# Optimization experiments

Measured on AMD Instinct MI355X. Metric: run time of the kernel, lower is better.

Reference implementation:

```python
import jax, jax.numpy as jnp
import numpy as np
from functools import partial

N_MAX = 10
M = 10
T = 0.5
SQRT_T = T ** 0.5
HIDDEN = 2048
LATENT = 128
STROKE = 5
B = 128
INPUT_DIM = LATENT + STROKE  # 133
OUT_DIM = 6 * M + 3          # 63


def setup_inputs() -> dict:
    key = jax.random.key(0)
    ks = jax.random.split(key, 10)
    def init(k, shape, fan_in):
        return jax.random.normal(k, shape, dtype=jnp.float32) * (1.0 / np.sqrt(fan_in))
    return {
        "z": jax.random.normal(ks[0], (B, LATENT), dtype=jnp.float32),
        "N_s": jax.random.randint(ks[1], (B,), 0, N_MAX),
        "fc_in_w": init(ks[2], (2 * HIDDEN, LATENT), LATENT),
        "fc_in_b": jnp.zeros((2 * HIDDEN,), jnp.float32),
        "W_ih": init(ks[3], (4 * HIDDEN, INPUT_DIM), INPUT_DIM),
        "W_hh": init(ks[4], (4 * HIDDEN, HIDDEN), HIDDEN),
        "b_ih": jnp.zeros((4 * HIDDEN,), jnp.float32),
        "b_hh": jnp.zeros((4 * HIDDEN,), jnp.float32),
        "proj_w": init(ks[5], (OUT_DIM, HIDDEN), HIDDEN),
        "proj_b": jnp.zeros((OUT_DIM,), jnp.float32),
    }


def reference(z, N_s, fc_in_w, fc_in_b, W_ih, W_hh, b_ih, b_hh, proj_w, proj_b):
    # initial hidden/cell from latent: tanh(fc_in(z)) split into (h, c)
    hc = jnp.tanh(z @ fc_in_w.T + fc_in_b)          # (B, 2H)
    h0, c0 = hc[:, :HIDDEN], hc[:, HIDDEN:]
    keys = jax.random.split(jax.random.key(42), N_MAX)
    stroke0 = jnp.tile(jnp.array([0., 0., 1., 0., 0.], z.dtype), (B, 1))
    empty = jnp.array([0., 0., 0., 0., 1.], z.dtype)
    eye3 = jnp.eye(3, dtype=z.dtype)

    def step(carry, inp):
        h, c, stroke = carry
        i, key = inp
        # ---- LSTM cell (PyTorch gate order i,f,g,o) ----
        x = jnp.concatenate([z, stroke], axis=1)                     # (B, 133)
        gates = x @ W_ih.T + b_ih + h @ W_hh.T + b_hh                # (B, 4H)
        ig, fg, gg, og = jnp.split(gates, 4, axis=1)
        c_new = jax.nn.sigmoid(fg) * c + jax.nn.sigmoid(ig) * jnp.tanh(gg)
        h_new = jax.nn.sigmoid(og) * jnp.tanh(c_new)
        out = h_new @ proj_w.T + proj_b                              # (B, 63)
        # ---- MDN parameter extraction ----
        mix = out[:, :6 * M].reshape(B, M, 6)                        # (B, M, 6)
        pi = jax.nn.softmax(mix[:, :, 0] / T, axis=1)                # (B, M)
        mux, muy = mix[:, :, 1], mix[:, :, 2]
        sx = jnp.exp(mix[:, :, 3]) * SQRT_T
        sy = jnp.exp(mix[:, :, 4]) * SQRT_T
        rho = jnp.tanh(mix[:, :, 5])
        pen = jax.nn.softmax(out[:, 6 * M:] / T, axis=1)             # (B, 3)
        # ---- categorical sampling via cumsum + searchsorted ----
        k1, k2, k3, k4 = jax.random.split(key, 4)
        u = jax.random.uniform(k1, (B,), dtype=z.dtype)
        rx = jax.random.normal(k2, (B,), dtype=z.dtype)
        ry = jax.random.normal(k3, (B,), dtype=z.dtype)
        u2 = jax.random.uniform(k4, (B,), dtype=z.dtype)
        idx = jnp.clip(jnp.sum(jnp.cumsum(pi, axis=1) < u[:, None], axis=1), 0, M - 1)
        take = lambda a: jnp.take_along_axis(a, idx[:, None], axis=1)[:, 0]
        mx, my = take(mux), take(muy)
        sxg, syg, rg = take(sx), take(sy), take(rho)
        ox = mx + sxg * rx
        oy = my + syg * (rg * ox + jnp.sqrt(1.0 - rg ** 2) * ry)
        pidx = jnp.clip(jnp.sum(jnp.cumsum(pen, axis=1) < u2[:, None], axis=1), 0, 2)
        nxt = jnp.concatenate([ox[:, None], oy[:, None], eye3[pidx]], axis=1)  # (B, 5)
        # finished sequences emit the empty stroke
        nxt = jnp.where((i > N_s)[:, None], empty, nxt)
        return (h_new, c_new, nxt), nxt

    _, strokes = jax.lax.scan(step, (h0, c0, stroke0), (jnp.arange(N_MAX), keys))
    return strokes  # (N_max, B, stroke_dim)
```

## Files before the change

### kernel.cpp

```cpp
#include <hip/hip_runtime.h>
#include <stdint.h>
#include <stddef.h>

#define HID 2048
#define NB 128
#define NG 8192
#define ODIM 63

typedef unsigned int u32;
typedef unsigned short u16;
typedef short bf16x8 __attribute__((ext_vector_type(8)));
typedef float f32x4 __attribute__((ext_vector_type(4)));

__device__ __forceinline__ u16 f2bf(float x) {
  u32 u = __float_as_uint(x);
  return (u16)((u + 0x7FFFu + ((u >> 16) & 1u)) >> 16);
}
__device__ __forceinline__ float bf2f(u16 b) {
  return __uint_as_float(((u32)b) << 16);
}

__device__ __forceinline__ void tf2x32(u32 k0, u32 k1, u32 x0, u32 x1,
                                       u32& o0, u32& o1) {
  u32 ks2 = k0 ^ k1 ^ 0x1BD11BDAu;
  x0 += k0; x1 += k1;
#define TF_ROTL(v,d) (((v)<<(d))|((v)>>(32-(d))))
#define TF_R(r) { x0 += x1; x1 = TF_ROTL(x1,r); x1 ^= x0; }
  TF_R(13) TF_R(15) TF_R(26) TF_R(6)
  x0 += k1;  x1 += ks2 + 1u;
  TF_R(17) TF_R(29) TF_R(16) TF_R(24)
  x0 += ks2; x1 += k0 + 2u;
  TF_R(13) TF_R(15) TF_R(26) TF_R(6)
  x0 += k0;  x1 += k1 + 3u;
  TF_R(17) TF_R(29) TF_R(16) TF_R(24)
  x0 += k1;  x1 += ks2 + 4u;
  TF_R(13) TF_R(15) TF_R(26) TF_R(6)
  x0 += ks2; x1 += k0 + 5u;
  o0 = x0; o1 = x1;
#undef TF_R
#undef TF_ROTL
}

__device__ __forceinline__ float unif01(u32 b) {
  return __uint_as_float((b >> 9) | 0x3f800000u) - 1.0f;
}

__device__ __forceinline__ float erfinv_xla(float x) {
  float t = x * x;
  float w = -log1pf(-t);
  float p;
  if (w < 5.0f) {
    w = w - 2.5f;
    p = 2.81022636e-08f;
    p = fmaf(p, w, 3.43273939e-07f);
    p = fmaf(p, w, -3.5233877e-06f);
    p = fmaf(p, w, -4.39150654e-06f);
    p = fmaf(p, w, 0.00021858087f);
    p = fmaf(p, w, -0.00125372503f);
    p = fmaf(p, w, -0.00417768164f);
    p = fmaf(p, w, 0.246640727f);
    p = fmaf(p, w, 1.50140941f);
  } else {
    w = sqrtf(w) - 3.0f;
    p = -0.000200214257f;
    p = fmaf(p, w, 0.000100950558f);
    p = fmaf(p, w, 0.00134934322f);
    p = fmaf(p, w, -0.00367342844f);
    p = fmaf(p, w, 0.00573950773f);
    p = fmaf(p, w, -0.0076224613f);
    p = fmaf(p, w, 0.00943887047f);
    p = fmaf(p, w, 1.00167406f);
    p = fmaf(p, w, 2.83297682f);
  }
  return p * x;
}

__device__ __forceinline__ float norm_from_bits(u32 b) {
  float f = unif01(b);
  float v = f * 2.0f + __uint_as_float(0xBF7FFFFFu);
  return __uint_as_float(0x3FB504F3u) * erfinv_xla(v);
}

__global__ void rand_kernel(float* __restrict__ u, float* __restrict__ rx,
                            float* __restrict__ ry, float* __restrict__ u2,
                            float* __restrict__ stroke) {
  const int i = blockIdx.x;
  const int l = threadIdx.x;
  if (i == 0) {
    stroke[l*5+0] = 0.f; stroke[l*5+1] = 0.f; stroke[l*5+2] = 1.f;
    stroke[l*5+3] = 0.f; stroke[l*5+4] = 0.f;
  }
  u32 ki0, ki1;
  tf2x32(0u, 42u, 0u, (u32)i, ki0, ki1);
  u32 k1a,k1b,k2a,k2b,k3a,k3b,k4a,k4b;
  tf2x32(ki0, ki1, 0u, 0u, k1a, k1b);
  tf2x32(ki0, ki1, 0u, 1u, k2a, k2b);
  tf2x32(ki0, ki1, 0u, 2u, k3a, k3b);
  tf2x32(ki0, ki1, 0u, 3u, k4a, k4b);
  u32 o0, o1;
  const u32 ul = (u32)l;
  tf2x32(k1a, k1b, 0u, ul, o0, o1);  u [i*NB + l] = unif01(o0 ^ o1);
  tf2x32(k2a, k2b, 0u, ul, o0, o1);  rx[i*NB + l] = norm_from_bits(o0 ^ o1);
  tf2x32(k3a, k3b, 0u, ul, o0, o1);  ry[i*NB + l] = norm_from_bits(o0 ^ o1);
  tf2x32(k4a, k4b, 0u, ul, o0, o1);  u2[i*NB + l] = unif01(o0 ^ o1);
}

__global__ __launch_bounds__(256) void w_split(const float* __restrict__ W,
                                               u16* __restrict__ Whi,
                                               u16* __restrict__ Wlo) {
  const int i8 = (blockIdx.x * 256 + threadIdx.x) * 8;
  float4 v0 = *(const float4*)&W[i8];
  float4 v1 = *(const float4*)&W[i8 + 4];
  float v[8] = {v0.x, v0.y, v0.z, v0.w, v1.x, v1.y, v1.z, v1.w};
  u32 hp[4], lp[4];
#pragma unroll
  for (int j = 0; j < 4; ++j) {
    u16 h0 = f2bf(v[2*j]),   l0 = f2bf(v[2*j]   - bf2f(h0));
    u16 h1 = f2bf(v[2*j+1]), l1 = f2bf(v[2*j+1] - bf2f(h1));
    hp[j] = (u32)h0 | ((u32)h1 << 16);
    lp[j] = (u32)l0 | ((u32)l1 << 16);
  }
  *(uint4*)&Whi[i8] = make_uint4(hp[0], hp[1], hp[2], hp[3]);
  *(uint4*)&Wlo[i8] = make_uint4(lp[0], lp[1], lp[2], lp[3]);
}

#define BM 64
#define BN 64
#define BK 16
__global__ __launch_bounds__(256) void gemm_bt(
    const float* __restrict__ A, const float* __restrict__ B,
    int K, int ldb, int N, int mode,
    const float* __restrict__ bias1, const float* __restrict__ bias2,
    float* __restrict__ C, float* __restrict__ C2,
    u16* __restrict__ Chi, u16* __restrict__ Clo)
{
  __shared__ float As[BK][BM];
  __shared__ float Bs[BK][BN];
  const int tid = threadIdx.x;
  const int bm = blockIdx.y * BM;
  const int bn = blockIdx.x * BN;
  const int lr = tid >> 2;
  const int lk = (tid & 3) << 2;
  const int ty = tid >> 4, tx = tid & 15;
  const int mo = ty << 2, no = tx << 2;
  const bool b_aligned = ((ldb & 3) == 0);
  float acc[4][4] = {{0.f,0.f,0.f,0.f},{0.f,0.f,0.f,0.f},{0.f,0.f,0.f,0.f},{0.f,0.f,0.f,0.f}};

  for (int k0 = 0; k0 < K; k0 += BK) {
    const float* ap = A + (size_t)(bm + lr) * K + (k0 + lk);
    float4 av = *(const float4*)ap;
    As[lk+0][lr] = av.x; As[lk+1][lr] = av.y; As[lk+2][lr] = av.z; As[lk+3][lr] = av.w;
    const float* bp = B + (size_t)(bn + lr) * ldb + (k0 + lk);
    float4 bv;
    if (b_aligned) { bv = *(const float4*)bp; }
    else { bv.x = bp[0]; bv.y = bp[1]; bv.z = bp[2]; bv.w = bp[3]; }
    Bs[lk+0][lr] = bv.x; Bs[lk+1][lr] = bv.y; Bs[lk+2][lr] = bv.z; Bs[lk+3][lr] = bv.w;
    __syncthreads();
#pragma unroll
    for (int k = 0; k < BK; ++k) {
      float4 a = *(const float4*)&As[k][mo];
      float4 b = *(const float4*)&Bs[k][no];
      acc[0][0] = fmaf(a.x, b.x, acc[0][0]);
      acc[0][1] = fmaf(a.x, b.y, acc[0][1]);
      acc[0][2] = fmaf(a.x, b.z, acc[0][2]);
      acc[0][3] = fmaf(a.x, b.w, acc[0][3]);
      acc[1][0] = fmaf(a.y, b.x, acc[1][0]);
      acc[1][1] = fmaf(a.y, b.y, acc[1][1]);
      acc[1][2] = fmaf(a.y, b.z, acc[1][2]);
      acc[1][3] = fmaf(a.y, b.w, acc[1][3]);
      acc[2][0] = fmaf(a.z, b.x, acc[2][0]);
      acc[2][1] = fmaf(a.z, b.y, acc[2][1]);
      acc[2][2] = fmaf(a.z, b.z, acc[2][2]);
      acc[2][3] = fmaf(a.z, b.w, acc[2][3]);
      acc[3][0] = fmaf(a.w, b.x, acc[3][0]);
      acc[3][1] = fmaf(a.w, b.y, acc[3][1]);
      acc[3][2] = fmaf(a.w, b.z, acc[3][2]);
      acc[3][3] = fmaf(a.w, b.w, acc[3][3]);
    }
    __syncthreads();
  }

  const int n0 = bn + no;
#pragma unroll
  for (int i = 0; i < 4; ++i) {
    const int m = bm + mo + i;
    if (mode == 1) {
      float4 r;
      r.x = tanhf(acc[i][0] + bias1[n0+0]);
      r.y = tanhf(acc[i][1] + bias1[n0+1]);
      r.z = tanhf(acc[i][2] + bias1[n0+2]);
      r.w = tanhf(acc[i][3] + bias1[n0+3]);
      if (n0 < HID) {
        *(float4*)&C[(size_t)m * HID + n0] = r;
        if (Chi) {
          float rv[4] = {r.x, r.y, r.z, r.w};
          u32 hp[2], lp[2];
#pragma unroll
          for (int j = 0; j < 2; ++j) {
            u16 h0 = f2bf(rv[2*j]),   l0 = f2bf(rv[2*j]   - bf2f(h0));
            u16 h1 = f2bf(rv[2*j+1]), l1 = f2bf(rv[2*j+1] - bf2f(h1));
            hp[j] = (u32)h0 | ((u32)h1 << 16);
            lp[j] = (u32)l0 | ((u32)l1 << 16);
          }
          *(uint2*)&Chi[(size_t)m * HID + n0] = make_uint2(hp[0], hp[1]);
          *(uint2*)&Clo[(size_t)m * HID + n0] = make_uint2(lp[0], lp[1]);
        }
      } else {
        *(float4*)&C2[(size_t)m * HID + (n0-HID)] = r;
      }
    } else {
      float4 r;
      r.x = acc[i][0] + bias1[n0+0] + bias2[n0+0];
      r.y = acc[i][1] + bias1[n0+1] + bias2[n0+1];
      r.z = acc[i][2] + bias1[n0+2] + bias2[n0+2];
      r.w = acc[i][3] + bias1[n0+3] + bias2[n0+3];
      *(float4*)&C[(size_t)m * N + n0] = r;
    }
  }
}

__global__ __launch_bounds__(256) void rec_mfma_lstm(
    const u16* __restrict__ hHi, const u16* __restrict__ hLo,
    const u16* __restrict__ WHi, const u16* __restrict__ WLo,
    const float* __restrict__ gz,
    const float* __restrict__ W_ih,
    const float* __restrict__ stroke,
    float* __restrict__ c,
    float* __restrict__ h_next,
    u16* __restrict__ hHiN, u16* __restrict__ hLoN)
{
  __shared__ float gt[4][32][33];
  const int tid = threadIdx.x;
  const int jc = blockIdx.x;
  const int mb = blockIdx.y;
  const int g  = tid >> 6;
  const int l  = tid & 63;
  const int lr = l & 15;
  const int lk = (l >> 4) * 8;

  f32x4 acc00 = {0.f,0.f,0.f,0.f}, acc01 = {0.f,0.f,0.f,0.f};
  f32x4 acc10 = {0.f,0.f,0.f,0.f}, acc11 = {0.f,0.f,0.f,0.f};

  const u16* pa0h = hHi + (size_t)(mb*32 +      lr) * HID + lk;
  const u16* pa1h = hHi + (size_t)(mb*32 + 16 + lr) * HID + lk;
  const u16* pa0l = hLo + (size_t)(mb*32 +      lr) * HID + lk;
  const u16* pa1l = hLo + (size_t)(mb*32 + 16 + lr) * HID + lk;
  const size_t bn0 = (size_t)(g*HID + jc*32 +      lr) * HID + lk;
  const size_t bn1 = (size_t)(g*HID + jc*32 + 16 + lr) * HID + lk;
  const u16* pb0h = WHi + bn0;
  const u16* pb1h = WHi + bn1;
  const u16* pb0l = WLo + bn0;
  const u16* pb1l = WLo + bn1;

#pragma unroll 2
  for (int k0 = 0; k0 < HID; k0 += 32) {
    bf16x8 a0h = *(const bf16x8*)(pa0h + k0);
    bf16x8 a1h = *(const bf16x8*)(pa1h + k0);
    bf16x8 a0l = *(const bf16x8*)(pa0l + k0);
    bf16x8 a1l = *(const bf16x8*)(pa1l + k0);
    bf16x8 b0h = *(const bf16x8*)(pb0h + k0);
    bf16x8 b1h = *(const bf16x8*)(pb1h + k0);
    bf16x8 b0l = *(const bf16x8*)(pb0l + k0);
    bf16x8 b1l = *(const bf16x8*)(pb1l + k0);
    acc00 = __builtin_amdgcn_mfma_f32_16x16x32_bf16(a0h, b0h, acc00, 0, 0, 0);
    acc00 = __builtin_amdgcn_mfma_f32_16x16x32_bf16(a0h, b0l, acc00, 0, 0, 0);
    acc00 = __builtin_amdgcn_mfma_f32_16x16x32_bf16(a0l, b0h, acc00, 0, 0, 0);
    acc01 = __builtin_amdgcn_mfma_f32_16x16x32_bf16(a0h, b1h, acc01, 0, 0, 0);
    acc01 = __builtin_amdgcn_mfma_f32_16x16x32_bf16(a0h, b1l, acc01, 0, 0, 0);
    acc01 = __builtin_amdgcn_mfma_f32_16x16x32_bf16(a0l, b1h, acc01, 0, 0, 0);
    acc10 = __builtin_amdgcn_mfma_f32_16x16x32_bf16(a1h, b0h, acc10, 0, 0, 0);
    acc10 = __builtin_amdgcn_mfma_f32_16x16x32_bf16(a1h, b0l, acc10, 0, 0, 0);
    acc10 = __builtin_amdgcn_mfma_f32_16x16x32_bf16(a1l, b0h, acc10, 0, 0, 0);
    acc11 = __builtin_amdgcn_mfma_f32_16x16x32_bf16(a1h, b1h, acc11, 0, 0, 0);
    acc11 = __builtin_amdgcn_mfma_f32_16x16x32_bf16(a1h, b1l, acc11, 0, 0, 0);
    acc11 = __builtin_amdgcn_mfma_f32_16x16x32_bf16(a1l, b1h, acc11, 0, 0, 0);
  }

  {
    const int rr = (l >> 4) * 4;
#pragma unroll
    for (int r = 0; r < 4; ++r) {
      gt[g][ 0 + rr + r][ 0 + lr] = acc00[r];
      gt[g][ 0 + rr + r][16 + lr] = acc01[r];
      gt[g][16 + rr + r][ 0 + lr] = acc10[r];
      gt[g][16 + rr + r][16 + lr] = acc11[r];
    }
  }
  __syncthreads();

  const int m  = tid >> 3;
  const int j4 = (tid & 7) * 4;
  const int gm = mb*32 + m;
  const int col = jc*32 + j4;
  float gv[4][4];
#pragma unroll
  for (int q = 0; q < 4; ++q) {
    float4 z4 = *(const float4*)&gz[(size_t)gm * NG + q * HID + col];
    gv[q][0] = z4.x + gt[q][m][j4+0];
    gv[q][1] = z4.y + gt[q][m][j4+1];
    gv[q][2] = z4.z + gt[q][m][j4+2];
    gv[q][3] = z4.w + gt[q][m][j4+3];
  }
  const float* st = stroke + gm*5;
  float s0 = st[0], s1 = st[1], s2 = st[2], s3 = st[3], s4 = st[4];
#pragma unroll
  for (int q = 0; q < 4; ++q) {
#pragma unroll
    for (int i = 0; i < 4; ++i) {
      const float* w = W_ih + (size_t)(q * HID + col + i) * 133 + 128;
      float t0 = gv[q][i];
      t0 = fmaf(s0, w[0], t0);
      t0 = fmaf(s1, w[1], t0);
      t0 = fmaf(s2, w[2], t0);
      t0 = fmaf(s3, w[3], t0);
      t0 = fmaf(s4, w[4], t0);
      gv[q][i] = t0;
    }
  }
  const size_t cidx = (size_t)gm * HID + col;
  float4 cv = *(float4*)&c[cidx];
  float cin[4] = {cv.x, cv.y, cv.z, cv.w};
  float hn[4], cn[4];
#pragma unroll
  for (int i = 0; i < 4; ++i) {
    float ig = 1.0f / (1.0f + expf(-gv[0][i]));
    float fg = 1.0f / (1.0f + expf(-gv[1][i]));
    float gg = tanhf(gv[2][i]);
    float og = 1.0f / (1.0f + expf(-gv[3][i]));
    cn[i] = fg * cin[i] + ig * gg;
    hn[i] = og * tanhf(cn[i]);
  }
  *(float4*)&c[cidx]      = make_float4(cn[0], cn[1], cn[2], cn[3]);
  *(float4*)&h_next[cidx] = make_float4(hn[0], hn[1], hn[2], hn[3]);
  u32 hp[2], lp[2];
#pragma unroll
  for (int j = 0; j < 2; ++j) {
    u16 h0 = f2bf(hn[2*j]),   l0 = f2bf(hn[2*j]   - bf2f(h0));
    u16 h1 = f2bf(hn[2*j+1]), l1 = f2bf(hn[2*j+1] - bf2f(h1));
    hp[j] = (u32)h0 | ((u32)h1 << 16);
    lp[j] = (u32)l0 | ((u32)l1 << 16);
  }
  *(uint2*)&hHiN[cidx] = make_uint2(hp[0], hp[1]);
  *(uint2*)&hLoN[cidx] = make_uint2(lp[0], lp[1]);
}

#define BK2 32
__global__ __launch_bounds__(256) void rec_gemm_lstm(
    const float* __restrict__ A, const float* __restrict__ W,
    const float* __restrict__ gz, const float* __restrict__ W_ih,
    const float* __restrict__ stroke, float* __restrict__ c,
    float* __restrict__ h_next)
{
  __shared__ float As[2][BK2][64];
  __shared__ float Bs[2][BK2][64];
  __shared__ float gt[64][68];
  const int tid = threadIdx.x;
  const int jc = blockIdx.x;
  const int bm = blockIdx.y * 64;
  const int j0 = jc * 16;
  const int sr = tid & 63;
  const int sk = (tid >> 6) << 3;
  const int brow = (sr >> 4) * HID + j0 + (sr & 15);
  const int mo = (tid >> 4) << 2;
  const int no = (tid & 15) << 2;
  float acc[4][4] = {{0.f,0.f,0.f,0.f},{0.f,0.f,0.f,0.f},{0.f,0.f,0.f,0.f},{0.f,0.f,0.f,0.f}};
  const float* abase = A + (size_t)(bm + sr) * HID + sk;
  const float* bbase = W + (size_t)brow * HID + sk;
#define STG(bi) do { \
    As[bi][sk+0][sr]=ra0.x; As[bi][sk+1][sr]=ra0.y; As[bi][sk+2][sr]=ra0.z; As[bi][sk+3][sr]=ra0.w; \
    As[bi][sk+4][sr]=ra1.x; As[bi][sk+5][sr]=ra1.y; As[bi][sk+6][sr]=ra1.z; As[bi][sk+7][sr]=ra1.w; \
    Bs[bi][sk+0][sr]=rb0.x; Bs[bi][sk+1][sr]=rb0.y; Bs[bi][sk+2][sr]=rb0.z; Bs[bi][sk+3][sr]=rb0.w; \
    Bs[bi][sk+4][sr]=rb1.x; Bs[bi][sk+5][sr]=rb1.y; Bs[bi][sk+6][sr]=rb1.z; Bs[bi][sk+7][sr]=rb1.w; \
  } while (0)
  float4 ra0 = *(const float4*)(abase);
  float4 ra1 = *(const float4*)(abase + 4);
  float4 rb0 = *(const float4*)(bbase);
  float4 rb1 = *(const float4*)(bbase + 4);
  STG(0);
  __syncthreads();
  int cur = 0;
  for (int t = 0; t < 64; ++t) {
    if (t < 63) {
      ra0 = *(const float4*)(abase + (t+1)*BK2);
      ra1 = *(const float4*)(abase + (t+1)*BK2 + 4);
      rb0 = *(const float4*)(bbase + (t+1)*BK2);
      rb1 = *(const float4*)(bbase + (t+1)*BK2 + 4);
    }
#pragma unroll
    for (int k = 0; k < BK2; ++k) {
      float4 a = *(const float4*)&As[cur][k][mo];
      float4 b = *(const float4*)&Bs[cur][k][no];
      acc[0][0] = fmaf(a.x, b.x, acc[0][0]);
      acc[0][1] = fmaf(a.x, b.y, acc[0][1]);
      acc[0][2] = fmaf(a.x, b.z, acc[0][2]);
      acc[0][3] = fmaf(a.x, b.w, acc[0][3]);
      acc[1][0] = fmaf(a.y, b.x, acc[1][0]);
      acc[1][1] = fmaf(a.y, b.y, acc[1][1]);
      acc[1][2] = fmaf(a.y, b.z, acc[1][2]);
      acc[1][3] = fmaf(a.y, b.w, acc[1][3]);
      acc[2][0] = fmaf(a.z, b.x, acc[2][0]);
      acc[2][1] = fmaf(a.z, b.y, acc[2][1]);
      acc[2][2] = fmaf(a.z, b.z, acc[2][2]);
      acc[2][3] = fmaf(a.z, b.w, acc[2][3]);
      acc[3][0] = fmaf(a.w, b.x, acc[3][0]);
      acc[3][1] = fmaf(a.w, b.y, acc[3][1]);
      acc[3][2] = fmaf(a.w, b.z, acc[3][2]);
      acc[3][3] = fmaf(a.w, b.w, acc[3][3]);
    }
    if (t < 63) STG(cur ^ 1);
    __syncthreads();
    cur ^= 1;
  }
#undef STG
  const int g = no >> 4;
#pragma unroll
  for (int i = 0; i < 4; ++i) {
    const int m = mo + i;
    float4 gzv = *(const float4*)&gz[(size_t)(bm + m) * NG + g * HID + j0 + (no & 15)];
    gt[m][no+0] = acc[i][0] + gzv.x;
    gt[m][no+1] = acc[i][1] + gzv.y;
    gt[m][no+2] = acc[i][2] + gzv.z;
    gt[m][no+3] = acc[i][3] + gzv.w;
  }
  __syncthreads();
#pragma unroll
  for (int p = 0; p < 4; ++p) {
    const int pid = p * 256 + tid;
    const int m  = pid >> 4;
    const int jj = pid & 15;
    const int gm = bm + m;
    const int col = j0 + jj;
    float gv[4];
    gv[0] = gt[m][jj];
    gv[1] = gt[m][16+jj];
    gv[2] = gt[m][32+jj];
    gv[3] = gt[m][48+jj];
    const float* st = stroke + gm*5;
    float s0 = st[0], s1 = st[1], s2 = st[2], s3 = st[3], s4 = st[4];
#pragma unroll
    for (int q = 0; q < 4; ++q) {
      const float* w = W_ih + (size_t)(q * HID + col) * 133 + 128;
      float t0 = gv[q];
      t0 = fmaf(s0, w[0], t0);
      t0 = fmaf(s1, w[1], t0);
      t0 = fmaf(s2, w[2], t0);
      t0 = fmaf(s3, w[3], t0);
      t0 = fmaf(s4, w[4], t0);
      gv[q] = t0;
    }
    float ig = 1.0f / (1.0f + expf(-gv[0]));
    float fg = 1.0f / (1.0f + expf(-gv[1]));
    float gg = tanhf(gv[2]);
    float og = 1.0f / (1.0f + expf(-gv[3]));
    const size_t idx = (size_t)gm * HID + col;
    float cn = fg * c[idx] + ig * gg;
    float hnv = og * tanhf(cn);
    c[idx] = cn;
    h_next[idx] = hnv;
  }
}

__global__ __launch_bounds__(256) void projsample(
    const float* __restrict__ h, const float* __restrict__ pw,
    const float* __restrict__ pb, const int* __restrict__ N_s,
    const float* __restrict__ u, const float* __restrict__ rx,
    const float* __restrict__ ry, const float* __restrict__ u2, int step,
    float* __restrict__ stroke, float* __restrict__ dout)
{
  __shared__ float hl[4*520];
  __shared__ float outs[64];
  const int b = blockIdx.x;
  const int t = threadIdx.x;
  const float* hp = h + (size_t)b * HID;
  {
    const int part = t >> 6;
    const int kk = (t * 8) & 511;
    float4 v0 = *(const float4*)&hp[t*8];
    float4 v1 = *(const float4*)&hp[t*8+4];
    *(float4*)&hl[part*520 + kk]     = v0;
    *(float4*)&hl[part*520 + kk + 4] = v1;
  }
  __syncthreads();
  if (t < 252) {
    const int n = t >> 2, part = t & 3;
    const float* wrow = pw + (size_t)n * HID + part * 512;
    const float* hh = hl + part * 520;
    float acc = 0.f;
#pragma unroll 4
    for (int k = 0; k < 512; k += 4) {
      float4 wv = *(const float4*)&wrow[k];
      float4 hv = *(const float4*)&hh[k];
      acc = fmaf(hv.x, wv.x, acc);
      acc = fmaf(hv.y, wv.y, acc);
      acc = fmaf(hv.z, wv.z, acc);
      acc = fmaf(hv.w, wv.w, acc);
    }
    acc += __shfl_xor(acc, 1);
    acc += __shfl_xor(acc, 2);
    if (part == 0) outs[n] = acc + pb[n];
  }
  __syncthreads();
  if (t == 0) {
    const float* o = outs;
    float xs[10];
    float mx = -3.402823466e+38f;
#pragma unroll
    for (int m = 0; m < 10; ++m) { xs[m] = o[6*m] * 2.0f; mx = fmaxf(mx, xs[m]); }
    float e[10]; float ssum = 0.f;
#pragma unroll
    for (int m = 0; m < 10; ++m) { e[m] = expf(xs[m] - mx); ssum += e[m]; }
    float uu = u[b];
    int cnt = 0; float csum = 0.f;
#pragma unroll
    for (int m = 0; m < 10; ++m) { csum += e[m] / ssum; cnt += (csum < uu) ? 1 : 0; }
    int idx = cnt > 9 ? 9 : cnt;
    float mux = o[6*idx+1], muy = o[6*idx+2];
    float sxg = expf(o[6*idx+3]) * __uint_as_float(0x3F3504F3u);
    float syg = expf(o[6*idx+4]) * __uint_as_float(0x3F3504F3u);
    float rg  = tanhf(o[6*idx+5]);
    float ox = mux + sxg * rx[b];
    float oy = muy + syg * (rg * ox + sqrtf(1.0f - rg*rg) * ry[b]);
    float p0 = o[60]*2.0f, p1 = o[61]*2.0f, p2 = o[62]*2.0f;
    float pmx = fmaxf(p0, fmaxf(p1, p2));
    float e0 = expf(p0-pmx), e1 = expf(p1-pmx), e2 = expf(p2-pmx);
    float es = e0+e1+e2;
    float uu2 = u2[b];
    int c2 = 0; float cs = 0.f;
    cs += e0/es; c2 += (cs < uu2) ? 1 : 0;
    cs += e1/es; c2 += (cs < uu2) ? 1 : 0;
    cs += e2/es; c2 += (cs < uu2) ? 1 : 0;
    int pidx = c2 > 2 ? 2 : c2;
    float nx0 = ox, nx1 = oy;
    float nx2 = (pidx==0)?1.f:0.f, nx3 = (pidx==1)?1.f:0.f, nx4 = (pidx==2)?1.f:0.f;
    if (step > N_s[b]) { nx0=0.f; nx1=0.f; nx2=0.f; nx3=0.f; nx4=1.f; }
    float* sp = stroke + b*5;
    sp[0]=nx0; sp[1]=nx1; sp[2]=nx2; sp[3]=nx3; sp[4]=nx4;
    float* dp = dout + b*5;
    dp[0]=nx0; dp[1]=nx1; dp[2]=nx2; dp[3]=nx3; dp[4]=nx4;
  }
}

extern "C" void kernel_launch(void* const* d_in, const int* in_sizes, int n_in,
                              void* d_out, int out_size, void* d_ws, size_t ws_size,
                              hipStream_t stream) {
  const float* z    = (const float*)d_in[0];
  const int*   N_s  = (const int*)  d_in[1];
  const float* fc_w = (const float*)d_in[2];
  const float* fc_b = (const float*)d_in[3];
  const float* W_ih = (const float*)d_in[4];
  const float* W_hh = (const float*)d_in[5];
  const float* b_ih = (const float*)d_in[6];
  const float* b_hh = (const float*)d_in[7];
  const float* pw   = (const float*)d_in[8];
  const float* pb   = (const float*)d_in[9];

  char* ws = (char*)d_ws;
  float* hA     = (float*)(ws + 0);
  float* c      = (float*)(ws + 1048576);
  float* gz     = (float*)(ws + 2097152);
  float* hB     = (float*)(ws + 6291456);
  float* u      = (float*)(ws + 10518528);
  float* rx     = (float*)(ws + 10523648);
  float* ry     = (float*)(ws + 10528768);
  float* u2     = (float*)(ws + 10533888);
  float* stroke = (float*)(ws + 10539008);
  u16*   Whi    = (u16*)(ws + 11534336);
  u16*   Wlo    = (u16*)(ws + 45088768);
  u16*   hHiA   = (u16*)(ws + 78643200);
  u16*   hLoA   = (u16*)(ws + 79167488);
  u16*   hHiB   = (u16*)(ws + 79691776);
  u16*   hLoB   = (u16*)(ws + 80216064);
  float* dout   = (float*)d_out;

  const bool fast = (ws_size >= 80740352ull);

  rand_kernel<<<dim3(10), dim3(128), 0, stream>>>(u, rx, ry, u2, stroke);
  gemm_bt<<<dim3(4096/BN, NB/BM), dim3(256), 0, stream>>>(
      z, fc_w, 128, 128, 4096, 1, fc_b, nullptr, hA, c,
      fast ? hHiA : nullptr, fast ? hLoA : nullptr);
  gemm_bt<<<dim3(NG/BN, NB/BM), dim3(256), 0, stream>>>(
      z, W_ih, 128, 133, NG, 2, b_ih, b_hh, gz, nullptr, nullptr, nullptr);

  if (fast) {
    w_split<<<dim3(8192), dim3(256), 0, stream>>>(W_hh, Whi, Wlo);
    u16* hhi[2] = { hHiA, hHiB };
    u16* hlo[2] = { hLoA, hLoB };
    float* hbuf[2] = { hA, hB };
    for (int s = 0; s < 10; ++s) {
      rec_mfma_lstm<<<dim3(64, 4), dim3(256), 0, stream>>>(
          hhi[s & 1], hlo[s & 1], Whi, Wlo, gz, W_ih, stroke, c,
          hbuf[(s + 1) & 1], hhi[(s + 1) & 1], hlo[(s + 1) & 1]);
      projsample<<<dim3(NB), dim3(256), 0, stream>>>(
          hbuf[(s + 1) & 1], pw, pb, N_s, u + s*NB, rx + s*NB, ry + s*NB,
          u2 + s*NB, s, stroke, dout + s*NB*5);
    }
  } else {
    float* hbuf[2] = { hA, hB };
    for (int s = 0; s < 10; ++s) {
      rec_gemm_lstm<<<dim3(HID/16, NB/64), dim3(256), 0, stream>>>(
          hbuf[s & 1], W_hh, gz, W_ih, stroke, c, hbuf[(s + 1) & 1]);
      projsample<<<dim3(NB), dim3(256), 0, stream>>>(
          hbuf[(s + 1) & 1], pw, pb, N_s, u + s*NB, rx + s*NB, ry + s*NB,
          u2 + s*NB, s, stroke, dout + s*NB*5);
    }
  }
}
```

Before: 1.020 ms.

## Retile recurrent MFMA LSTM kernel to 16-row blocks with 8 waves and prefetch

The recurrent LSTM step kernel now launches 512 blocks of 512 threads instead of 256 blocks of 256. Each block covers 16 batch rows by 32 hidden columns across four gates, with one wave per gate and column half. The K loop is fully unrolled with register double-buffering of the next A/B fragments. The three split-precision products go into separate accumulators to break MFMA dependency chains. This aims to raise occupancy and hide global load latency, but each W_hh tile is now reloaded by twice as many blocks, and the epilogue switches from vectorised to scalar per-element stores.

Measured after the change: 1.501 ms. 1.47x slower.

```diff
diff --git a/kernel.cpp b/kernel.cpp
--- a/kernel.cpp
+++ b/kernel.cpp
@@ -219,7 +219,7 @@
   }
 }
 
-__global__ __launch_bounds__(256) void rec_mfma_lstm(
+__global__ __launch_bounds__(512, 4) void rec_mfma_lstm(
     const u16* __restrict__ hHi, const u16* __restrict__ hLo,
     const u16* __restrict__ WHi, const u16* __restrict__ WLo,
     const float* __restrict__ gz,
@@ -229,119 +229,97 @@
     float* __restrict__ h_next,
     u16* __restrict__ hHiN, u16* __restrict__ hLoN)
 {
-  __shared__ float gt[4][32][33];
+  __shared__ float gt[4][16][33];
   const int tid = threadIdx.x;
-  const int jc = blockIdx.x;
-  const int mb = blockIdx.y;
-  const int g  = tid >> 6;
+  const int mb = blockIdx.x >> 6;
+  const int jc = blockIdx.x & 63;
+  const int w  = tid >> 6;
+  const int g  = w >> 1;
+  const int nh = w & 1;
   const int l  = tid & 63;
   const int lr = l & 15;
   const int lk = (l >> 4) * 8;
 
-  f32x4 acc00 = {0.f,0.f,0.f,0.f}, acc01 = {0.f,0.f,0.f,0.f};
-  f32x4 acc10 = {0.f,0.f,0.f,0.f}, acc11 = {0.f,0.f,0.f,0.f};
-
-  const u16* pa0h = hHi + (size_t)(mb*32 +      lr) * HID + lk;
-  const u16* pa1h = hHi + (size_t)(mb*32 + 16 + lr) * HID + lk;
-  const u16* pa0l = hLo + (size_t)(mb*32 +      lr) * HID + lk;
-  const u16* pa1l = hLo + (size_t)(mb*32 + 16 + lr) * HID + lk;
-  const size_t bn0 = (size_t)(g*HID + jc*32 +      lr) * HID + lk;
-  const size_t bn1 = (size_t)(g*HID + jc*32 + 16 + lr) * HID + lk;
-  const u16* pb0h = WHi + bn0;
-  const u16* pb1h = WHi + bn1;
-  const u16* pb0l = WLo + bn0;
-  const u16* pb1l = WLo + bn1;
-
-#pragma unroll 2
-  for (int k0 = 0; k0 < HID; k0 += 32) {
-    bf16x8 a0h = *(const bf16x8*)(pa0h + k0);
-    bf16x8 a1h = *(const bf16x8*)(pa1h + k0);
-    bf16x8 a0l = *(const bf16x8*)(pa0l + k0);
-    bf16x8 a1l = *(const bf16x8*)(pa1l + k0);
-    bf16x8 b0h = *(const bf16x8*)(pb0h + k0);
-    bf16x8 b1h = *(const bf16x8*)(pb1h + k0);
-    bf16x8 b0l = *(const bf16x8*)(pb0l + k0);
-    bf16x8 b1l = *(const bf16x8*)(pb1l + k0);
-    acc00 = __builtin_amdgcn_mfma_f32_16x16x32_bf16(a0h, b0h, acc00, 0, 0, 0);
-    acc00 = __builtin_amdgcn_mfma_f32_16x16x32_bf16(a0h, b0l, acc00, 0, 0, 0);
-    acc00 = __builtin_amdgcn_mfma_f32_16x16x32_bf16(a0l, b0h, acc00, 0, 0, 0);
-    acc01 = __builtin_amdgcn_mfma_f32_16x16x32_bf16(a0h, b1h, acc01, 0, 0, 0);
-    acc01 = __builtin_amdgcn_mfma_f32_16x16x32_bf16(a0h, b1l, acc01, 0, 0, 0);
-    acc01 = __builtin_amdgcn_mfma_f32_16x16x32_bf16(a0l, b1h, acc01, 0, 0, 0);
-    acc10 = __builtin_amdgcn_mfma_f32_16x16x32_bf16(a1h, b0h, acc10, 0, 0, 0);
-    acc10 = __builtin_amdgcn_mfma_f32_16x16x32_bf16(a1h, b0l, acc10, 0, 0, 0);
-    acc10 = __builtin_amdgcn_mfma_f32_16x16x32_bf16(a1l, b0h, acc10, 0, 0, 0);
-    acc11 = __builtin_amdgcn_mfma_f32_16x16x32_bf16(a1h, b1h, acc11, 0, 0, 0);
-    acc11 = __builtin_amdgcn_mfma_f32_16x16x32_bf16(a1h, b1l, acc11, 0, 0, 0);
-    acc11 = __builtin_amdgcn_mfma_f32_16x16x32_bf16(a1l, b1h, acc11, 0, 0, 0);
+  f32x4 ahh = {0.f,0.f,0.f,0.f}, ahl = {0.f,0.f,0.f,0.f}, alh = {0.f,0.f,0.f,0.f};
+
+  const u16* pah = hHi + (size_t)(mb*16 + lr) * HID + lk;
+  const u16* pal = hLo + (size_t)(mb*16 + lr) * HID + lk;
+  const size_t bn = (size_t)(g*HID + jc*32 + nh*16 + lr) * HID + lk;
+  const u16* pbh = WHi + bn;
+  const u16* pbl = WLo + bn;
+
+  bf16x8 a0h = *(const bf16x8*)(pah);
+  bf16x8 a0l = *(const bf16x8*)(pal);
+  bf16x8 b0h = *(const bf16x8*)(pbh);
+  bf16x8 b0l = *(const bf16x8*)(pbl);
+  bf16x8 a1h, a1l, b1h, b1l;
+
+#pragma unroll
+  for (int k0 = 0; k0 < 64; ++k0) {
+    if ((k0 & 1) == 0) {
+      if (k0 < 63) {
+        a1h = *(const bf16x8*)(pah + (k0+1)*32);
+        a1l = *(const bf16x8*)(pal + (k0+1)*32);
+        b1h = *(const bf16x8*)(pbh + (k0+1)*32);
+        b1l = *(const bf16x8*)(pbl + (k0+1)*32);
+      }
+      ahh = __builtin_amdgcn_mfma_f32_16x16x32_bf16(a0h, b0h, ahh, 0, 0, 0);
+      ahl = __builtin_amdgcn_mfma_f32_16x16x32_bf16(a0h, b0l, ahl, 0, 0, 0);
+      alh = __builtin_amdgcn_mfma_f32_16x16x32_bf16(a0l, b0h, alh, 0, 0, 0);
+    } else {
+      if (k0 < 63) {
+        a0h = *(const bf16x8*)(pah + (k0+1)*32);
+        a0l = *(const bf16x8*)(pal + (k0+1)*32);
+        b0h = *(const bf16x8*)(pbh + (k0+1)*32);
+        b0l = *(const bf16x8*)(pbl + (k0+1)*32);
+      }
+      ahh = __builtin_amdgcn_mfma_f32_16x16x32_bf16(a1h, b1h, ahh, 0, 0, 0);
+      ahl = __builtin_amdgcn_mfma_f32_16x16x32_bf16(a1h, b1l, ahl, 0, 0, 0);
+      alh = __builtin_amdgcn_mfma_f32_16x16x32_bf16(a1l, b1h, alh, 0, 0, 0);
+    }
   }
 
   {
     const int rr = (l >> 4) * 4;
 #pragma unroll
-    for (int r = 0; r < 4; ++r) {
-      gt[g][ 0 + rr + r][ 0 + lr] = acc00[r];
-      gt[g][ 0 + rr + r][16 + lr] = acc01[r];
-      gt[g][16 + rr + r][ 0 + lr] = acc10[r];
-      gt[g][16 + rr + r][16 + lr] = acc11[r];
-    }
+    for (int r = 0; r < 4; ++r)
+      gt[g][rr + r][nh*16 + lr] = ahh[r] + ahl[r] + alh[r];
   }
   __syncthreads();
 
-  const int m  = tid >> 3;
-  const int j4 = (tid & 7) * 4;
-  const int gm = mb*32 + m;
-  const int col = jc*32 + j4;
-  float gv[4][4];
-#pragma unroll
-  for (int q = 0; q < 4; ++q) {
-    float4 z4 = *(const float4*)&gz[(size_t)gm * NG + q * HID + col];
-    gv[q][0] = z4.x + gt[q][m][j4+0];
-    gv[q][1] = z4.y + gt[q][m][j4+1];
-    gv[q][2] = z4.z + gt[q][m][j4+2];
-    gv[q][3] = z4.w + gt[q][m][j4+3];
-  }
+  const int m = tid >> 5;
+  const int j = tid & 31;
+  const int gm  = mb*16 + m;
+  const int col = jc*32 + j;
+  float gv[4];
+#pragma unroll
+  for (int q = 0; q < 4; ++q)
+    gv[q] = gz[(size_t)gm * NG + q * HID + col] + gt[q][m][j];
   const float* st = stroke + gm*5;
   float s0 = st[0], s1 = st[1], s2 = st[2], s3 = st[3], s4 = st[4];
 #pragma unroll
   for (int q = 0; q < 4; ++q) {
-#pragma unroll
-    for (int i = 0; i < 4; ++i) {
-      const float* w = W_ih + (size_t)(q * HID + col + i) * 133 + 128;
-      float t0 = gv[q][i];
-      t0 = fmaf(s0, w[0], t0);
-      t0 = fmaf(s1, w[1], t0);
-      t0 = fmaf(s2, w[2], t0);
-      t0 = fmaf(s3, w[3], t0);
-      t0 = fmaf(s4, w[4], t0);
-      gv[q][i] = t0;
-    }
-  }
+    const float* wp = W_ih + (size_t)(q * HID + col) * 133 + 128;
+    float t0 = gv[q];
+    t0 = fmaf(s0, wp[0], t0);
+    t0 = fmaf(s1, wp[1], t0);
+    t0 = fmaf(s2, wp[2], t0);
+    t0 = fmaf(s3, wp[3], t0);
+    t0 = fmaf(s4, wp[4], t0);
+    gv[q] = t0;
+  }
+  float ig = 1.0f / (1.0f + expf(-gv[0]));
+  float fg = 1.0f / (1.0f + expf(-gv[1]));
+  float gg = tanhf(gv[2]);
+  float og = 1.0f / (1.0f + expf(-gv[3]));
   const size_t cidx = (size_t)gm * HID + col;
-  float4 cv = *(float4*)&c[cidx];
-  float cin[4] = {cv.x, cv.y, cv.z, cv.w};
-  float hn[4], cn[4];
-#pragma unroll
-  for (int i = 0; i < 4; ++i) {
-    float ig = 1.0f / (1.0f + expf(-gv[0][i]));
-    float fg = 1.0f / (1.0f + expf(-gv[1][i]));
-    float gg = tanhf(gv[2][i]);
-    float og = 1.0f / (1.0f + expf(-gv[3][i]));
-    cn[i] = fg * cin[i] + ig * gg;
-    hn[i] = og * tanhf(cn[i]);
-  }
-  *(float4*)&c[cidx]      = make_float4(cn[0], cn[1], cn[2], cn[3]);
-  *(float4*)&h_next[cidx] = make_float4(hn[0], hn[1], hn[2], hn[3]);
-  u32 hp[2], lp[2];
-#pragma unroll
-  for (int j = 0; j < 2; ++j) {
-    u16 h0 = f2bf(hn[2*j]),   l0 = f2bf(hn[2*j]   - bf2f(h0));
-    u16 h1 = f2bf(hn[2*j+1]), l1 = f2bf(hn[2*j+1] - bf2f(h1));
-    hp[j] = (u32)h0 | ((u32)h1 << 16);
-    lp[j] = (u32)l0 | ((u32)l1 << 16);
-  }
-  *(uint2*)&hHiN[cidx] = make_uint2(hp[0], hp[1]);
-  *(uint2*)&hLoN[cidx] = make_uint2(lp[0], lp[1]);
+  float cn = fg * c[cidx] + ig * gg;
+  float hn = og * tanhf(cn);
+  c[cidx] = cn;
+  h_next[cidx] = hn;
+  u16 hh = f2bf(hn);
+  hHiN[cidx] = hh;
+  hLoN[cidx] = f2bf(hn - bf2f(hh));
 }
 
 #define BK2 32
@@ -439,13 +417,13 @@
     float s0 = st[0], s1 = st[1], s2 = st[2], s3 = st[3], s4 = st[4];
 #pragma unroll
     for (int q = 0; q < 4; ++q) {
-      const float* w = W_ih + (size_t)(q * HID + col) * 133 + 128;
+      const float* wp = W_ih + (size_t)(q * HID + col) * 133 + 128;
       float t0 = gv[q];
-      t0 = fmaf(s0, w[0], t0);
-      t0 = fmaf(s1, w[1], t0);
-      t0 = fmaf(s2, w[2], t0);
-      t0 = fmaf(s3, w[3], t0);
-      t0 = fmaf(s4, w[4], t0);
+      t0 = fmaf(s0, wp[0], t0);
+      t0 = fmaf(s1, wp[1], t0);
+      t0 = fmaf(s2, wp[2], t0);
+      t0 = fmaf(s3, wp[3], t0);
+      t0 = fmaf(s4, wp[4], t0);
       gv[q] = t0;
     }
     float ig = 1.0f / (1.0f + expf(-gv[0]));
@@ -587,7 +565,7 @@
     u16* hlo[2] = { hLoA, hLoB };
     float* hbuf[2] = { hA, hB };
     for (int s = 0; s < 10; ++s) {
-      rec_mfma_lstm<<<dim3(64, 4), dim3(256), 0, stream>>>(
+      rec_mfma_lstm<<<dim3(512), dim3(512), 0, stream>>>(
           hhi[s & 1], hlo[s & 1], Whi, Wlo, gz, W_ih, stroke, c,
           hbuf[(s + 1) & 1], hhi[(s + 1) & 1], hlo[(s + 1) & 1]);
       projsample<<<dim3(NB), dim3(256), 0, stream>>>(
```
